# Kernel tuning notes

Hardware: AMD Instinct MI355X
Metric: run time of the kernel (lower is better)

The kernel has to match this reference:

```python
import jax, jax.numpy as jnp
import numpy as np

B, T, D, H, L = 64, 512, 512, 512, 2


def setup_inputs() -> dict:
    key = jax.random.key(0)
    ks = jax.random.split(key, 9)
    std = 1.0 / np.sqrt(H)
    u = lambda k, shape: jax.random.uniform(k, shape, jnp.float32, -std, std)
    return {
        "x": jax.random.normal(ks[0], (B, T, D), jnp.float32),
        "Wx0": u(ks[1], (4 * H, D)), "bx0": u(ks[2], (4 * H,)),
        "Wh0": u(ks[3], (4 * H, H)), "bh0": u(ks[4], (4 * H,)),
        "Wx1": u(ks[5], (4 * H, H)), "bx1": u(ks[6], (4 * H,)),
        "Wh1": u(ks[7], (4 * H, H)), "bh1": u(ks[8], (4 * H,)),
    }


def _lstm_layer(x_seq, Wx, bx, Wh, bh):
    # x_seq: [T, B, D_in] -> hidden sequence [T, B, H]
    h0 = jnp.zeros((x_seq.shape[1], Wh.shape[1]), x_seq.dtype)
    c0 = jnp.zeros_like(h0)
    # precompute input projections for all steps (one big GEMM)
    xg = jnp.einsum('tbd,gd->tbg', x_seq, Wx) + bx + bh  # [T, B, 4H]

    def step(carry, xg_t):
        h, c = carry
        gates = xg_t + h @ Wh.T
        f, i, g, o = jnp.split(gates, 4, axis=1)
        f = jax.nn.sigmoid(f)
        i = jax.nn.sigmoid(i)
        g = jnp.tanh(g)
        o = jax.nn.sigmoid(o)
        c = f * c + i * g
        h = o * jnp.tanh(c)
        return (h, c), h

    (_, _), hs = jax.lax.scan(step, (h0, c0), xg)
    return hs


def reference(x, Wx0, bx0, Wh0, bh0, Wx1, bx1, Wh1, bh1):
    xs = jnp.transpose(x, (1, 0, 2))  # [T, B, D]
    h1 = _lstm_layer(xs, Wx0, bx0, Wh0, bh0)   # [T, B, H]
    h2 = _lstm_layer(h1, Wx1, bx1, Wh1, bh1)   # [T, B, H]
    return h2[-1]  # last hidden state of top layer: [B, H]
```

## Files before the change

kernel.cpp:

```cpp
#include <hip/hip_runtime.h>
#include <hip/hip_bf16.h>
#include <stdint.h>

#define T_STEPS 512
#define BATCH   64
#define HID     512
#define DIN     512
#define G4      2048
#define HBLK_T  32768
#define SENT8   0xFFFFFFFFFFFFFFFFull

typedef __attribute__((ext_vector_type(8))) short bf16x8;
typedef __attribute__((ext_vector_type(4))) float f32x4;
typedef __attribute__((ext_vector_type(4))) unsigned short us4;
typedef unsigned long long ull;

static __device__ __forceinline__ unsigned short f2bf(float f) {
  union { float f; unsigned u; } v; v.f = f;
  unsigned r = v.u + 0x7FFFu + ((v.u >> 16) & 1u);
  return (unsigned short)(r >> 16);
}
static __device__ __forceinline__ float bf2f(unsigned short s) {
  union { unsigned u; float f; } v; v.u = ((unsigned)s) << 16;
  return v.f;
}
static __device__ __forceinline__ float sigf(float x) { return 1.f / (1.f + __expf(-x)); }
static __device__ __forceinline__ float tanh_fast(float x) {
  x = fminf(15.f, fmaxf(-15.f, x));
  float e = __expf(2.f * x);
  return (e - 1.f) / (e + 1.f);
}

__global__ void cvt_f32_bf16(const float* __restrict__ src, unsigned short* __restrict__ dst, long n) {
  long i = (long)blockIdx.x * blockDim.x + threadIdx.x;
  long st = (long)gridDim.x * blockDim.x;
  for (; i < n; i += st) dst[i] = f2bf(src[i]);
}

__global__ __launch_bounds__(256) void proj_kernel(
    const float* __restrict__ x,
    const unsigned short* __restrict__ Wb,
    const float* __restrict__ ba,
    const float* __restrict__ bb,
    unsigned short* __restrict__ xg) {
  __shared__ unsigned short xt[64 * 512];
  const int t   = blockIdx.x;
  const int tid = threadIdx.x;

  for (int i = 0; i < 16; ++i) {
    const int c    = i * 256 + tid;
    const int b    = c >> 6;
    const int col8 = c & 63;
    const float* src = x + ((long)b * T_STEPS + t) * DIN + col8 * 8;
    f32x4 v0 = *(const f32x4*)(src);
    f32x4 v1 = *(const f32x4*)(src + 4);
    union { unsigned short s[8]; bf16x8 v; } u;
    #pragma unroll
    for (int e = 0; e < 4; ++e) { u.s[e] = f2bf(v0[e]); u.s[4 + e] = f2bf(v1[e]); }
    const int byteoff = b * 1024 + ((col8 * 16) ^ ((b & 7) << 4));
    *(bf16x8*)((char*)xt + byteoff) = u.v;
  }
  __syncthreads();

  const int wv   = tid >> 6;
  const int lane = tid & 63;
  const int n16  = lane & 15;
  const int q    = lane >> 4;
  const int kof  = q * 8;

  for (int gt = 0; gt < 32; ++gt) {
    const int g0 = wv * 512 + gt * 16;
    const unsigned short* ap = Wb + (long)(g0 + n16) * DIN + kof;
    f32x4 acc[4];
    #pragma unroll
    for (int nb = 0; nb < 4; ++nb) acc[nb] = (f32x4){0.f, 0.f, 0.f, 0.f};
    #pragma unroll
    for (int kk = 0; kk < 16; ++kk) {
      bf16x8 a = *(const bf16x8*)(ap + kk * 32);
      const int colb = (kof + kk * 32) * 2;
      #pragma unroll
      for (int nb = 0; nb < 4; ++nb) {
        const int row = nb * 16 + n16;
        bf16x8 bv = *(const bf16x8*)((const char*)xt + row * 1024 + (colb ^ ((row & 7) << 4)));
        acc[nb] = __builtin_amdgcn_mfma_f32_16x16x32_bf16(a, bv, acc[nb], 0, 0, 0);
      }
    }
    const int m0 = q * 4;
    #pragma unroll
    for (int r = 0; r < 4; ++r) {
      const int g = g0 + m0 + r;
      const float bv = ba[g] + bb[g];
      long base = ((long)t * G4 + g) * BATCH + n16;
      xg[base +  0] = f2bf(acc[0][r] + bv);
      xg[base + 16] = f2bf(acc[1][r] + bv);
      xg[base + 32] = f2bf(acc[2][r] + bv);
      xg[base + 48] = f2bf(acc[3][r] + bv);
    }
  }
}

__global__ __launch_bounds__(128, 1) void fused_rec(
    const float* __restrict__ Wh0,
    const float* __restrict__ Wx1,
    const float* __restrict__ Wh1,
    const float* __restrict__ bx1, const float* __restrict__ bh1,
    const unsigned short* __restrict__ xg0,
    unsigned short* __restrict__ hseq1,
    unsigned short* __restrict__ hseq2,
    float* __restrict__ out,
    int T) {
  __shared__ unsigned short whl0[32 * 512];
  __shared__ unsigned short whl1[32 * 1024];
  __shared__ __align__(16) unsigned short ring[2 * 64 * 128];
  __shared__ __align__(16) unsigned short hsc[2][128];
  __shared__ int l0_wr, l1_rd;

  const int bid  = blockIdx.x;
  const int gq   = bid & 3;
  const int j    = bid >> 2;
  const int wv   = threadIdx.x >> 6;
  const int lane = threadIdx.x & 63;
  const int hidbase = j * 8;
  const int n16  = lane & 15;
  const int q    = lane >> 4;
  const int kof  = q * 8;
  const int bloc = q * 4;
  const int rr0 = n16, rr1 = 16 + n16;
  const int grow0 = (rr0 >> 3) * HID + hidbase + (rr0 & 7);
  const int grow1 = (rr1 >> 3) * HID + hidbase + (rr1 & 7);
  const int rdbase = gq * 128 + n16 * 8;
  const int myblk  = (j * 4 + gq) * 128;
  const int rsw    = (lane & 7) << 4;

  if (threadIdx.x == 0) { l0_wr = 0; l1_rd = 0; }

  auto cv8 = [](const float* s) -> bf16x8 {
    f32x4 a = *(const f32x4*)s, b = *(const f32x4*)(s + 4);
    union { unsigned short u[8]; bf16x8 v; } w;
    #pragma unroll
    for (int e = 0; e < 4; ++e) { w.u[e] = f2bf(a[e]); w.u[4 + e] = f2bf(b[e]); }
    return w.v;
  };
  if (wv == 0) {
    for (int r = 0; r < 32; ++r) {
      const long grow = (long)(r >> 3) * HID + hidbase + (r & 7);
      bf16x8 v = cv8(Wh0 + grow * HID + lane * 8);
      *(bf16x8*)((char*)whl0 + r * 1024 + ((lane * 16) ^ ((r & 7) << 4))) = v;
    }
  } else {
    for (int r = 0; r < 32; ++r) {
      const long grow = (long)(r >> 3) * HID + hidbase + (r & 7);
      bf16x8 va = cv8(Wx1 + grow * HID + lane * 8);
      bf16x8 vb = cv8(Wh1 + grow * HID + lane * 8);
      const int rb = r * 2048;
      *(bf16x8*)((char*)whl1 + rb + ((lane * 16) ^ ((r & 7) << 4))) = va;
      *(bf16x8*)((char*)whl1 + rb + ((1024 + lane * 16) ^ ((r & 7) << 4))) = vb;
    }
  }
  __syncthreads();

  if (wv == 0) {
    float c4[4] = {0.f, 0.f, 0.f, 0.f};
    for (int t = 0; t < T; ++t) {
      us4 xv0 = *(const us4*)(xg0 + ((long)t * G4 + grow0) * BATCH + gq * 16 + bloc);
      us4 xv1 = *(const us4*)(xg0 + ((long)t * G4 + grow1) * BATCH + gq * 16 + bloc);

      ull lo[16], hi[16];
      f32x4 acc0 = {0.f,0.f,0.f,0.f}, acc1 = {0.f,0.f,0.f,0.f};
      if (t > 0) {
        const ull* hp = (const ull*)(hseq1 + (long)(t - 1) * HBLK_T + rdbase);
        int bad;
        do {
          bad = 0;
          #pragma unroll
          for (int kk = 0; kk < 16; ++kk) {
            const int boff = (kk * 4 + q) * 128;
            lo[kk] = __hip_atomic_load(hp + boff,     __ATOMIC_RELAXED, __HIP_MEMORY_SCOPE_AGENT);
            hi[kk] = __hip_atomic_load(hp + boff + 1, __ATOMIC_RELAXED, __HIP_MEMORY_SCOPE_AGENT);
          }
          #pragma unroll
          for (int kk = 0; kk < 16; ++kk)
            bad |= (lo[kk] == SENT8) | (hi[kk] == SENT8);
        } while (__any(bad));
        #pragma unroll
        for (int kk = 0; kk < 16; ++kk) {
          union { ull qq[2]; bf16x8 v; } u; u.qq[0] = lo[kk]; u.qq[1] = hi[kk];
          const int colb = (kof + kk * 32) * 2;
          bf16x8 b0 = *(const bf16x8*)((const char*)whl0 + rr0 * 1024 + (colb ^ ((rr0 & 7) << 4)));
          bf16x8 b1 = *(const bf16x8*)((const char*)whl0 + rr1 * 1024 + (colb ^ ((rr1 & 7) << 4)));
          acc0 = __builtin_amdgcn_mfma_f32_16x16x32_bf16(u.v, b0, acc0, 0, 0, 0);
          acc1 = __builtin_amdgcn_mfma_f32_16x16x32_bf16(u.v, b1, acc1, 0, 0, 0);
        }
      }
      #pragma unroll
      for (int r = 0; r < 4; ++r) { acc0[r] += bf2f(xv0[r]); acc1[r] += bf2f(xv1[r]); }

      f32x4 o0, o1;
      #pragma unroll
      for (int r = 0; r < 4; ++r) {
        o0[r] = __shfl_xor(acc0[r], 8, 64);
        o1[r] = __shfl_xor(acc1[r], 8, 64);
      }
      if (n16 < 8) {
        #pragma unroll
        for (int r = 0; r < 4; ++r) {
          const float fg = sigf(acc0[r]);
          const float ig = sigf(o0[r]);
          const float gg = tanh_fast(acc1[r]);
          const float og = sigf(o1[r]);
          const float cn = fg * c4[r] + ig * gg;
          c4[r] = cn;
          const float h = og * tanh_fast(cn);
          *(unsigned short*)((char*)hsc[0] + (bloc + r) * 16 + n16 * 2) = f2bf(h);
        }
      }
      asm volatile("s_waitcnt lgkmcnt(0)" ::: "memory");
      if (lane < 32) {
        ull v8 = *(const ull*)((const char*)hsc[0] + lane * 8);
        ull* dst = (ull*)(hseq1 + (long)t * HBLK_T + myblk) + lane;
        __hip_atomic_store(dst, v8, __ATOMIC_RELAXED, __HIP_MEMORY_SCOPE_AGENT);
      }
      if (t > 0) {
        while (__hip_atomic_load(&l1_rd, __ATOMIC_RELAXED, __HIP_MEMORY_SCOPE_WORKGROUP) < t - 2) {}
        __builtin_amdgcn_sched_barrier(0);
        char* slot = (char*)ring + ((t - 1) & 1) * 16384 + lane * 256;
        #pragma unroll
        for (int kk = 0; kk < 16; ++kk) {
          union { ull qq[2]; bf16x8 v; } u; u.qq[0] = lo[kk]; u.qq[1] = hi[kk];
          *(bf16x8*)(slot + ((kk * 16) ^ rsw)) = u.v;
        }
        asm volatile("s_waitcnt lgkmcnt(0)" ::: "memory");
        __builtin_amdgcn_sched_barrier(0);
        if (lane == 0)
          __hip_atomic_store(&l0_wr, t, __ATOMIC_RELAXED, __HIP_MEMORY_SCOPE_WORKGROUP);
      }
    }
    {
      const ull* hp = (const ull*)(hseq1 + (long)(T - 1) * HBLK_T + rdbase);
      ull lo[16], hi[16];
      int bad;
      do {
        bad = 0;
        #pragma unroll
        for (int kk = 0; kk < 16; ++kk) {
          const int boff = (kk * 4 + q) * 128;
          lo[kk] = __hip_atomic_load(hp + boff,     __ATOMIC_RELAXED, __HIP_MEMORY_SCOPE_AGENT);
          hi[kk] = __hip_atomic_load(hp + boff + 1, __ATOMIC_RELAXED, __HIP_MEMORY_SCOPE_AGENT);
        }
        #pragma unroll
        for (int kk = 0; kk < 16; ++kk)
          bad |= (lo[kk] == SENT8) | (hi[kk] == SENT8);
      } while (__any(bad));
      while (__hip_atomic_load(&l1_rd, __ATOMIC_RELAXED, __HIP_MEMORY_SCOPE_WORKGROUP) < T - 2) {}
      __builtin_amdgcn_sched_barrier(0);
      char* slot = (char*)ring + ((T - 1) & 1) * 16384 + lane * 256;
      #pragma unroll
      for (int kk = 0; kk < 16; ++kk) {
        union { ull qq[2]; bf16x8 v; } u; u.qq[0] = lo[kk]; u.qq[1] = hi[kk];
        *(bf16x8*)(slot + ((kk * 16) ^ rsw)) = u.v;
      }
      asm volatile("s_waitcnt lgkmcnt(0)" ::: "memory");
      __builtin_amdgcn_sched_barrier(0);
      if (lane == 0)
        __hip_atomic_store(&l0_wr, T, __ATOMIC_RELAXED, __HIP_MEMORY_SCOPE_WORKGROUP);
    }
  } else {
    float c4[4] = {0.f, 0.f, 0.f, 0.f};
    const float b0v = bx1[grow0] + bh1[grow0];
    const float b1v = bx1[grow1] + bh1[grow1];
    for (int t = 0; t < T; ++t) {
      ull lb[16], hb[16];
      const ull* pb = (const ull*)(hseq2 + (long)(t - 1) * HBLK_T + rdbase);
      if (t > 0) {
        #pragma unroll
        for (int kk = 0; kk < 16; ++kk) {
          const int boff = (kk * 4 + q) * 128;
          lb[kk] = __hip_atomic_load(pb + boff,     __ATOMIC_RELAXED, __HIP_MEMORY_SCOPE_AGENT);
          hb[kk] = __hip_atomic_load(pb + boff + 1, __ATOMIC_RELAXED, __HIP_MEMORY_SCOPE_AGENT);
        }
      }
      while (__hip_atomic_load(&l0_wr, __ATOMIC_RELAXED, __HIP_MEMORY_SCOPE_WORKGROUP) < t + 1) {}
      __builtin_amdgcn_sched_barrier(0);
      bf16x8 ra[16];
      const char* slot = (const char*)ring + (t & 1) * 16384 + lane * 256;
      #pragma unroll
      for (int kk = 0; kk < 16; ++kk)
        ra[kk] = *(const bf16x8*)(slot + ((kk * 16) ^ rsw));
      asm volatile("s_waitcnt lgkmcnt(0)" ::: "memory");
      __builtin_amdgcn_sched_barrier(0);
      if (lane == 0)
        __hip_atomic_store(&l1_rd, t + 1, __ATOMIC_RELAXED, __HIP_MEMORY_SCOPE_WORKGROUP);
      f32x4 acc0 = {0.f,0.f,0.f,0.f}, acc1 = {0.f,0.f,0.f,0.f};
      #pragma unroll
      for (int kk = 0; kk < 16; ++kk) {
        const int colb = (kof + kk * 32) * 2;
        bf16x8 b0 = *(const bf16x8*)((const char*)whl1 + rr0 * 2048 + (colb ^ ((rr0 & 7) << 4)));
        bf16x8 b1 = *(const bf16x8*)((const char*)whl1 + rr1 * 2048 + (colb ^ ((rr1 & 7) << 4)));
        acc0 = __builtin_amdgcn_mfma_f32_16x16x32_bf16(ra[kk], b0, acc0, 0, 0, 0);
        acc1 = __builtin_amdgcn_mfma_f32_16x16x32_bf16(ra[kk], b1, acc1, 0, 0, 0);
      }
      if (t > 0) {
        for (;;) {
          int bad = 0;
          #pragma unroll
          for (int kk = 0; kk < 16; ++kk) bad |= (lb[kk] == SENT8) | (hb[kk] == SENT8);
          if (!__any(bad)) break;
          #pragma unroll
          for (int kk = 0; kk < 16; ++kk) {
            const int boff = (kk * 4 + q) * 128;
            lb[kk] = __hip_atomic_load(pb + boff,     __ATOMIC_RELAXED, __HIP_MEMORY_SCOPE_AGENT);
            hb[kk] = __hip_atomic_load(pb + boff + 1, __ATOMIC_RELAXED, __HIP_MEMORY_SCOPE_AGENT);
          }
        }
        #pragma unroll
        for (int kk = 0; kk < 16; ++kk) {
          union { ull qq[2]; bf16x8 v; } u; u.qq[0] = lb[kk]; u.qq[1] = hb[kk];
          const int colb = 1024 + (kof + kk * 32) * 2;
          bf16x8 b0 = *(const bf16x8*)((const char*)whl1 + rr0 * 2048 + (colb ^ ((rr0 & 7) << 4)));
          bf16x8 b1 = *(const bf16x8*)((const char*)whl1 + rr1 * 2048 + (colb ^ ((rr1 & 7) << 4)));
          acc0 = __builtin_amdgcn_mfma_f32_16x16x32_bf16(u.v, b0, acc0, 0, 0, 0);
          acc1 = __builtin_amdgcn_mfma_f32_16x16x32_bf16(u.v, b1, acc1, 0, 0, 0);
        }
      }
      #pragma unroll
      for (int r = 0; r < 4; ++r) { acc0[r] += b0v; acc1[r] += b1v; }

      f32x4 o0, o1;
      #pragma unroll
      for (int r = 0; r < 4; ++r) {
        o0[r] = __shfl_xor(acc0[r], 8, 64);
        o1[r] = __shfl_xor(acc1[r], 8, 64);
      }
      if (n16 < 8) {
        const int hid = hidbase + n16;
        #pragma unroll
        for (int r = 0; r < 4; ++r) {
          const float fg = sigf(acc0[r]);
          const float ig = sigf(o0[r]);
          const float gg = tanh_fast(acc1[r]);
          const float og = sigf(o1[r]);
          const float cn = fg * c4[r] + ig * gg;
          c4[r] = cn;
          const float h = og * tanh_fast(cn);
          *(unsigned short*)((char*)hsc[1] + (bloc + r) * 16 + n16 * 2) = f2bf(h);
          if (t == T - 1) out[(long)(gq * 16 + bloc + r) * HID + hid] = h;
        }
      }
      asm volatile("s_waitcnt lgkmcnt(0)" ::: "memory");
      if (lane < 32) {
        ull v8 = *(const ull*)((const char*)hsc[1] + lane * 8);
        ull* dst = (ull*)(hseq2 + (long)t * HBLK_T + myblk) + lane;
        __hip_atomic_store(dst, v8, __ATOMIC_RELAXED, __HIP_MEMORY_SCOPE_AGENT);
      }
    }
  }
}

extern "C" void kernel_launch(void* const* d_in, const int* in_sizes, int n_in,
                              void* d_out, int out_size, void* d_ws, size_t ws_size,
                              hipStream_t stream) {
  const float* x   = (const float*)d_in[0];
  const float* Wx0 = (const float*)d_in[1];
  const float* bx0 = (const float*)d_in[2];
  const float* Wh0 = (const float*)d_in[3];
  const float* bh0 = (const float*)d_in[4];
  const float* Wx1 = (const float*)d_in[5];
  const float* bx1 = (const float*)d_in[6];
  const float* Wh1 = (const float*)d_in[7];
  const float* bh1 = (const float*)d_in[8];

  char* ws = (char*)d_ws;
  size_t off = 0;
  auto alloc = [&](size_t bytes) -> char* {
    char* p = ws + off; off += (bytes + 255) & ~(size_t)255; return p;
  };
  unsigned short* xg    = (unsigned short*)alloc((size_t)T_STEPS * G4 * BATCH * 2);
  unsigned short* hseq1 = (unsigned short*)alloc((size_t)T_STEPS * HBLK_T * 2);
  unsigned short* hseq2 = (unsigned short*)alloc((size_t)T_STEPS * HBLK_T * 2);
  unsigned short* Wx0b  = (unsigned short*)alloc((size_t)G4 * DIN * 2);

  hipMemsetAsync(hseq1, 0xFF, (size_t)T_STEPS * HBLK_T * 2, stream);
  hipMemsetAsync(hseq2, 0xFF, (size_t)T_STEPS * HBLK_T * 2, stream);

  cvt_f32_bf16<<<1024, 256, 0, stream>>>(Wx0, Wx0b, (long)G4 * DIN);

  proj_kernel<<<T_STEPS, 256, 0, stream>>>(x, Wx0b, bx0, bh0, xg);
  fused_rec<<<256, 128, 0, stream>>>(Wh0, Wx1, Wh1, bx1, bh1,
                                     xg, hseq1, hseq2, (float*)d_out, T_STEPS);
}
```

Baseline: 2.087 ms.

## Transpose MFMA operands, store h directly, forward layer-1 ring earlier

Swaps the MFMA A/B operands so each lane's accumulator holds four consecutive hidden units for one batch row. That lets the h values be packed and stored straight to global memory without the shared-memory staging buffer, and the gate exchange becomes a single xor-32 shuffle. Layer 0 now writes the ring slot for layer 1 right after polling h, before its own matmul, which shortens layer 1's wait. Polling also re-reads only the words that still hold the sentinel. The x-gate loads become strided scalar loads, which may cost extra memory transactions.

```diff
diff --git a/kernel.cpp b/kernel.cpp
--- a/kernel.cpp
+++ b/kernel.cpp
@@ -14,6 +14,11 @@
 typedef __attribute__((ext_vector_type(4))) float f32x4;
 typedef __attribute__((ext_vector_type(4))) unsigned short us4;
 typedef unsigned long long ull;
+
+#define AGLD(p) __hip_atomic_load((p), __ATOMIC_RELAXED, __HIP_MEMORY_SCOPE_AGENT)
+#define AGST(p, v) __hip_atomic_store((p), (v), __ATOMIC_RELAXED, __HIP_MEMORY_SCOPE_AGENT)
+#define WGLD(p) __hip_atomic_load((p), __ATOMIC_RELAXED, __HIP_MEMORY_SCOPE_WORKGROUP)
+#define WGST(p, v) __hip_atomic_store((p), (v), __ATOMIC_RELAXED, __HIP_MEMORY_SCOPE_WORKGROUP)
 
 static __device__ __forceinline__ unsigned short f2bf(float f) {
   union { float f; unsigned u; } v; v.f = f;
@@ -112,7 +117,6 @@
   __shared__ unsigned short whl0[32 * 512];
   __shared__ unsigned short whl1[32 * 1024];
   __shared__ __align__(16) unsigned short ring[2 * 64 * 128];
-  __shared__ __align__(16) unsigned short hsc[2][128];
   __shared__ int l0_wr, l1_rd;
 
   const int bid  = blockIdx.x;
@@ -124,13 +128,11 @@
   const int n16  = lane & 15;
   const int q    = lane >> 4;
   const int kof  = q * 8;
-  const int bloc = q * 4;
   const int rr0 = n16, rr1 = 16 + n16;
-  const int grow0 = (rr0 >> 3) * HID + hidbase + (rr0 & 7);
-  const int grow1 = (rr1 >> 3) * HID + hidbase + (rr1 & 7);
   const int rdbase = gq * 128 + n16 * 8;
   const int myblk  = (j * 4 + gq) * 128;
   const int rsw    = (lane & 7) << 4;
+  const int gofs0  = (q >> 1) * 512 + hidbase + (q & 1) * 4;
 
   if (threadIdx.x == 0) { l0_wr = 0; l1_rd = 0; }
 
@@ -162,46 +164,65 @@
   if (wv == 0) {
     float c4[4] = {0.f, 0.f, 0.f, 0.f};
     for (int t = 0; t < T; ++t) {
-      us4 xv0 = *(const us4*)(xg0 + ((long)t * G4 + grow0) * BATCH + gq * 16 + bloc);
-      us4 xv1 = *(const us4*)(xg0 + ((long)t * G4 + grow1) * BATCH + gq * 16 + bloc);
-
+      const unsigned short* xp = xg0 + ((long)t * G4 + gofs0) * BATCH + gq * 16 + n16;
+      unsigned short xs0[4], xs1[4];
+      #pragma unroll
+      for (int r = 0; r < 4; ++r) {
+        xs0[r] = xp[r * BATCH];
+        xs1[r] = xp[(1024 + r) * BATCH];
+      }
       ull lo[16], hi[16];
-      f32x4 acc0 = {0.f,0.f,0.f,0.f}, acc1 = {0.f,0.f,0.f,0.f};
       if (t > 0) {
         const ull* hp = (const ull*)(hseq1 + (long)(t - 1) * HBLK_T + rdbase);
+        #pragma unroll
+        for (int kk = 0; kk < 16; ++kk) { lo[kk] = SENT8; hi[kk] = SENT8; }
         int bad;
         do {
-          bad = 0;
           #pragma unroll
           for (int kk = 0; kk < 16; ++kk) {
             const int boff = (kk * 4 + q) * 128;
-            lo[kk] = __hip_atomic_load(hp + boff,     __ATOMIC_RELAXED, __HIP_MEMORY_SCOPE_AGENT);
-            hi[kk] = __hip_atomic_load(hp + boff + 1, __ATOMIC_RELAXED, __HIP_MEMORY_SCOPE_AGENT);
+            if (lo[kk] == SENT8) lo[kk] = AGLD(hp + boff);
+            if (hi[kk] == SENT8) hi[kk] = AGLD(hp + boff + 1);
           }
+          bad = 0;
           #pragma unroll
           for (int kk = 0; kk < 16; ++kk)
             bad |= (lo[kk] == SENT8) | (hi[kk] == SENT8);
         } while (__any(bad));
+        while (WGLD(&l1_rd) < t - 2) {}
+        asm volatile("" ::: "memory");
+        char* slot = (char*)ring + ((t - 1) & 1) * 16384 + lane * 256;
+        #pragma unroll
+        for (int kk = 0; kk < 16; ++kk) {
+          union { ull qq[2]; bf16x8 v; } u; u.qq[0] = lo[kk]; u.qq[1] = hi[kk];
+          *(bf16x8*)(slot + ((kk * 16) ^ rsw)) = u.v;
+        }
+        asm volatile("s_waitcnt lgkmcnt(0)" ::: "memory");
+        if (lane == 0) WGST(&l0_wr, t);
+      }
+      f32x4 acc0 = {0.f,0.f,0.f,0.f}, acc1 = {0.f,0.f,0.f,0.f};
+      if (t > 0) {
         #pragma unroll
         for (int kk = 0; kk < 16; ++kk) {
           union { ull qq[2]; bf16x8 v; } u; u.qq[0] = lo[kk]; u.qq[1] = hi[kk];
           const int colb = (kof + kk * 32) * 2;
-          bf16x8 b0 = *(const bf16x8*)((const char*)whl0 + rr0 * 1024 + (colb ^ ((rr0 & 7) << 4)));
-          bf16x8 b1 = *(const bf16x8*)((const char*)whl0 + rr1 * 1024 + (colb ^ ((rr1 & 7) << 4)));
-          acc0 = __builtin_amdgcn_mfma_f32_16x16x32_bf16(u.v, b0, acc0, 0, 0, 0);
-          acc1 = __builtin_amdgcn_mfma_f32_16x16x32_bf16(u.v, b1, acc1, 0, 0, 0);
-        }
-      }
-      #pragma unroll
-      for (int r = 0; r < 4; ++r) { acc0[r] += bf2f(xv0[r]); acc1[r] += bf2f(xv1[r]); }
+          bf16x8 a0 = *(const bf16x8*)((const char*)whl0 + rr0 * 1024 + (colb ^ ((rr0 & 7) << 4)));
+          bf16x8 a1 = *(const bf16x8*)((const char*)whl0 + rr1 * 1024 + (colb ^ ((rr1 & 7) << 4)));
+          acc0 = __builtin_amdgcn_mfma_f32_16x16x32_bf16(a0, u.v, acc0, 0, 0, 0);
+          acc1 = __builtin_amdgcn_mfma_f32_16x16x32_bf16(a1, u.v, acc1, 0, 0, 0);
+        }
+      }
+      #pragma unroll
+      for (int r = 0; r < 4; ++r) { acc0[r] += bf2f(xs0[r]); acc1[r] += bf2f(xs1[r]); }
 
       f32x4 o0, o1;
       #pragma unroll
       for (int r = 0; r < 4; ++r) {
-        o0[r] = __shfl_xor(acc0[r], 8, 64);
-        o1[r] = __shfl_xor(acc1[r], 8, 64);
-      }
-      if (n16 < 8) {
+        o0[r] = __shfl_xor(acc0[r], 32, 64);
+        o1[r] = __shfl_xor(acc1[r], 32, 64);
+      }
+      if (q < 2) {
+        us4 hb4;
         #pragma unroll
         for (int r = 0; r < 4; ++r) {
           const float fg = sigf(acc0[r]);
@@ -210,49 +231,33 @@
           const float og = sigf(o1[r]);
           const float cn = fg * c4[r] + ig * gg;
           c4[r] = cn;
-          const float h = og * tanh_fast(cn);
-          *(unsigned short*)((char*)hsc[0] + (bloc + r) * 16 + n16 * 2) = f2bf(h);
-        }
-      }
-      asm volatile("s_waitcnt lgkmcnt(0)" ::: "memory");
-      if (lane < 32) {
-        ull v8 = *(const ull*)((const char*)hsc[0] + lane * 8);
-        ull* dst = (ull*)(hseq1 + (long)t * HBLK_T + myblk) + lane;
-        __hip_atomic_store(dst, v8, __ATOMIC_RELAXED, __HIP_MEMORY_SCOPE_AGENT);
-      }
-      if (t > 0) {
-        while (__hip_atomic_load(&l1_rd, __ATOMIC_RELAXED, __HIP_MEMORY_SCOPE_WORKGROUP) < t - 2) {}
-        __builtin_amdgcn_sched_barrier(0);
-        char* slot = (char*)ring + ((t - 1) & 1) * 16384 + lane * 256;
-        #pragma unroll
-        for (int kk = 0; kk < 16; ++kk) {
-          union { ull qq[2]; bf16x8 v; } u; u.qq[0] = lo[kk]; u.qq[1] = hi[kk];
-          *(bf16x8*)(slot + ((kk * 16) ^ rsw)) = u.v;
-        }
-        asm volatile("s_waitcnt lgkmcnt(0)" ::: "memory");
-        __builtin_amdgcn_sched_barrier(0);
-        if (lane == 0)
-          __hip_atomic_store(&l0_wr, t, __ATOMIC_RELAXED, __HIP_MEMORY_SCOPE_WORKGROUP);
+          hb4[r] = f2bf(og * tanh_fast(cn));
+        }
+        union { us4 v; ull u; } pk; pk.v = hb4;
+        ull* dst = (ull*)(hseq1 + (long)t * HBLK_T + myblk) + n16 * 2 + q;
+        AGST(dst, pk.u);
       }
     }
     {
       const ull* hp = (const ull*)(hseq1 + (long)(T - 1) * HBLK_T + rdbase);
       ull lo[16], hi[16];
+      #pragma unroll
+      for (int kk = 0; kk < 16; ++kk) { lo[kk] = SENT8; hi[kk] = SENT8; }
       int bad;
       do {
+        #pragma unroll
+        for (int kk = 0; kk < 16; ++kk) {
+          const int boff = (kk * 4 + q) * 128;
+          if (lo[kk] == SENT8) lo[kk] = AGLD(hp + boff);
+          if (hi[kk] == SENT8) hi[kk] = AGLD(hp + boff + 1);
+        }
         bad = 0;
-        #pragma unroll
-        for (int kk = 0; kk < 16; ++kk) {
-          const int boff = (kk * 4 + q) * 128;
-          lo[kk] = __hip_atomic_load(hp + boff,     __ATOMIC_RELAXED, __HIP_MEMORY_SCOPE_AGENT);
-          hi[kk] = __hip_atomic_load(hp + boff + 1, __ATOMIC_RELAXED, __HIP_MEMORY_SCOPE_AGENT);
-        }
         #pragma unroll
         for (int kk = 0; kk < 16; ++kk)
           bad |= (lo[kk] == SENT8) | (hi[kk] == SENT8);
       } while (__any(bad));
-      while (__hip_atomic_load(&l1_rd, __ATOMIC_RELAXED, __HIP_MEMORY_SCOPE_WORKGROUP) < T - 2) {}
-      __builtin_amdgcn_sched_barrier(0);
+      while (WGLD(&l1_rd) < T - 2) {}
+      asm volatile("" ::: "memory");
       char* slot = (char*)ring + ((T - 1) & 1) * 16384 + lane * 256;
       #pragma unroll
       for (int kk = 0; kk < 16; ++kk) {
@@ -260,14 +265,16 @@
         *(bf16x8*)(slot + ((kk * 16) ^ rsw)) = u.v;
       }
       asm volatile("s_waitcnt lgkmcnt(0)" ::: "memory");
-      __builtin_amdgcn_sched_barrier(0);
-      if (lane == 0)
-        __hip_atomic_store(&l0_wr, T, __ATOMIC_RELAXED, __HIP_MEMORY_SCOPE_WORKGROUP);
+      if (lane == 0) WGST(&l0_wr, T);
     }
   } else {
     float c4[4] = {0.f, 0.f, 0.f, 0.f};
-    const float b0v = bx1[grow0] + bh1[grow0];
-    const float b1v = bx1[grow1] + bh1[grow1];
+    float bv0[4], bv1[4];
+    #pragma unroll
+    for (int r = 0; r < 4; ++r) {
+      bv0[r] = bx1[gofs0 + r] + bh1[gofs0 + r];
+      bv1[r] = bx1[gofs0 + 1024 + r] + bh1[gofs0 + 1024 + r];
+    }
     for (int t = 0; t < T; ++t) {
       ull lb[16], hb[16];
       const ull* pb = (const ull*)(hseq2 + (long)(t - 1) * HBLK_T + rdbase);
@@ -275,12 +282,12 @@
         #pragma unroll
         for (int kk = 0; kk < 16; ++kk) {
           const int boff = (kk * 4 + q) * 128;
-          lb[kk] = __hip_atomic_load(pb + boff,     __ATOMIC_RELAXED, __HIP_MEMORY_SCOPE_AGENT);
-          hb[kk] = __hip_atomic_load(pb + boff + 1, __ATOMIC_RELAXED, __HIP_MEMORY_SCOPE_AGENT);
-        }
-      }
-      while (__hip_atomic_load(&l0_wr, __ATOMIC_RELAXED, __HIP_MEMORY_SCOPE_WORKGROUP) < t + 1) {}
-      __builtin_amdgcn_sched_barrier(0);
+          lb[kk] = AGLD(pb + boff);
+          hb[kk] = AGLD(pb + boff + 1);
+        }
+      }
+      while (WGLD(&l0_wr) < t + 1) {}
+      asm volatile("" ::: "memory");
       bf16x8 ra[16];
       const char* slot = (const char*)ring + (t & 1) * 16384 + lane * 256;
       #pragma unroll
@@ -288,16 +295,15 @@
         ra[kk] = *(const bf16x8*)(slot + ((kk * 16) ^ rsw));
       asm volatile("s_waitcnt lgkmcnt(0)" ::: "memory");
       __builtin_amdgcn_sched_barrier(0);
-      if (lane == 0)
-        __hip_atomic_store(&l1_rd, t + 1, __ATOMIC_RELAXED, __HIP_MEMORY_SCOPE_WORKGROUP);
+      if (lane == 0) WGST(&l1_rd, t + 1);
       f32x4 acc0 = {0.f,0.f,0.f,0.f}, acc1 = {0.f,0.f,0.f,0.f};
       #pragma unroll
       for (int kk = 0; kk < 16; ++kk) {
         const int colb = (kof + kk * 32) * 2;
-        bf16x8 b0 = *(const bf16x8*)((const char*)whl1 + rr0 * 2048 + (colb ^ ((rr0 & 7) << 4)));
-        bf16x8 b1 = *(const bf16x8*)((const char*)whl1 + rr1 * 2048 + (colb ^ ((rr1 & 7) << 4)));
-        acc0 = __builtin_amdgcn_mfma_f32_16x16x32_bf16(ra[kk], b0, acc0, 0, 0, 0);
-        acc1 = __builtin_amdgcn_mfma_f32_16x16x32_bf16(ra[kk], b1, acc1, 0, 0, 0);
+        bf16x8 a0 = *(const bf16x8*)((const char*)whl1 + rr0 * 2048 + (colb ^ ((rr0 & 7) << 4)));
+        bf16x8 a1 = *(const bf16x8*)((const char*)whl1 + rr1 * 2048 + (colb ^ ((rr1 & 7) << 4)));
+        acc0 = __builtin_amdgcn_mfma_f32_16x16x32_bf16(a0, ra[kk], acc0, 0, 0, 0);
+        acc1 = __builtin_amdgcn_mfma_f32_16x16x32_bf16(a1, ra[kk], acc1, 0, 0, 0);
       }
       if (t > 0) {
         for (;;) {
@@ -308,31 +314,31 @@
           #pragma unroll
           for (int kk = 0; kk < 16; ++kk) {
             const int boff = (kk * 4 + q) * 128;
-            lb[kk] = __hip_atomic_load(pb + boff,     __ATOMIC_RELAXED, __HIP_MEMORY_SCOPE_AGENT);
-            hb[kk] = __hip_atomic_load(pb + boff + 1, __ATOMIC_RELAXED, __HIP_MEMORY_SCOPE_AGENT);
+            if (lb[kk] == SENT8) lb[kk] = AGLD(pb + boff);
+            if (hb[kk] == SENT8) hb[kk] = AGLD(pb + boff + 1);
           }
         }
         #pragma unroll
         for (int kk = 0; kk < 16; ++kk) {
           union { ull qq[2]; bf16x8 v; } u; u.qq[0] = lb[kk]; u.qq[1] = hb[kk];
           const int colb = 1024 + (kof + kk * 32) * 2;
-          bf16x8 b0 = *(const bf16x8*)((const char*)whl1 + rr0 * 2048 + (colb ^ ((rr0 & 7) << 4)));
-          bf16x8 b1 = *(const bf16x8*)((const char*)whl1 + rr1 * 2048 + (colb ^ ((rr1 & 7) << 4)));
-          acc0 = __builtin_amdgcn_mfma_f32_16x16x32_bf16(u.v, b0, acc0, 0, 0, 0);
-          acc1 = __builtin_amdgcn_mfma_f32_16x16x32_bf16(u.v, b1, acc1, 0, 0, 0);
-        }
-      }
-      #pragma unroll
-      for (int r = 0; r < 4; ++r) { acc0[r] += b0v; acc1[r] += b1v; }
+          bf16x8 a0 = *(const bf16x8*)((const char*)whl1 + rr0 * 2048 + (colb ^ ((rr0 & 7) << 4)));
+          bf16x8 a1 = *(const bf16x8*)((const char*)whl1 + rr1 * 2048 + (colb ^ ((rr1 & 7) << 4)));
+          acc0 = __builtin_amdgcn_mfma_f32_16x16x32_bf16(a0, u.v, acc0, 0, 0, 0);
+          acc1 = __builtin_amdgcn_mfma_f32_16x16x32_bf16(a1, u.v, acc1, 0, 0, 0);
+        }
+      }
+      #pragma unroll
+      for (int r = 0; r < 4; ++r) { acc0[r] += bv0[r]; acc1[r] += bv1[r]; }
 
       f32x4 o0, o1;
       #pragma unroll
       for (int r = 0; r < 4; ++r) {
-        o0[r] = __shfl_xor(acc0[r], 8, 64);
-        o1[r] = __shfl_xor(acc1[r], 8, 64);
-      }
-      if (n16 < 8) {
-        const int hid = hidbase + n16;
+        o0[r] = __shfl_xor(acc0[r], 32, 64);
+        o1[r] = __shfl_xor(acc1[r], 32, 64);
+      }
+      if (q < 2) {
+        us4 hb4;
         #pragma unroll
         for (int r = 0; r < 4; ++r) {
           const float fg = sigf(acc0[r]);
@@ -342,15 +348,13 @@
           const float cn = fg * c4[r] + ig * gg;
           c4[r] = cn;
           const float h = og * tanh_fast(cn);
-          *(unsigned short*)((char*)hsc[1] + (bloc + r) * 16 + n16 * 2) = f2bf(h);
-          if (t == T - 1) out[(long)(gq * 16 + bloc + r) * HID + hid] = h;
-        }
-      }
-      asm volatile("s_waitcnt lgkmcnt(0)" ::: "memory");
-      if (lane < 32) {
-        ull v8 = *(const ull*)((const char*)hsc[1] + lane * 8);
-        ull* dst = (ull*)(hseq2 + (long)t * HBLK_T + myblk) + lane;
-        __hip_atomic_store(dst, v8, __ATOMIC_RELAXED, __HIP_MEMORY_SCOPE_AGENT);
+          hb4[r] = f2bf(h);
+          if (t == T - 1)
+            out[(long)(gq * 16 + n16) * HID + hidbase + q * 4 + r] = h;
+        }
+        union { us4 v; ull u; } pk; pk.v = hb4;
+        ull* dst = (ull*)(hseq2 + (long)t * HBLK_T + myblk) + n16 * 2 + q;
+        AGST(dst, pk.u);
       }
     }
   }
```

Result: no change. 2.097 ms (+0.5%).
